# Kernel tuning notes

Hardware: AMD Instinct MI355X
Metric: run time of the kernel (lower is better)

## Reference

```python
import jax, jax.numpy as jnp
import numpy as np

B = 2048


def _maxpool2(x):
    return jax.lax.reduce_window(x, -jnp.inf, jax.lax.max,
                                 (1, 1, 2, 2), (1, 1, 2, 2), 'VALID')


def setup_inputs() -> dict:
    key = jax.random.key(0)
    ks = jax.random.split(key, 7)
    return {
        'x': jax.random.normal(ks[0], (B, 3, 32, 32), dtype=jnp.float32),
        'conv_w': jax.random.normal(ks[1], (45, 1, 5, 5), dtype=jnp.float32),
        'conv_b': jax.random.normal(ks[2], (45,), dtype=jnp.float32) * 0.1,
        'tree_w': jax.random.normal(ks[3], (1, 16, 15, 3, 7, 7, 2, 2), dtype=jnp.float32),
        'tree_b': jax.random.normal(ks[4], (1, 16, 3, 7), dtype=jnp.float32),
        'fc_w': jax.random.normal(ks[5], (10, 336), dtype=jnp.float32),
        'fc_b': jax.random.normal(ks[6], (10,), dtype=jnp.float32) * 0.1,
    }


def reference(x, conv_w, conv_b, tree_w, tree_b, fc_w, fc_b):
    # grouped conv: in=3, groups=3, out=45, kernel 5x5, VALID -> (B,45,28,28)
    out = jax.lax.conv_general_dilated(
        x, conv_w, window_strides=(1, 1), padding='VALID',
        dimension_numbers=('NCHW', 'OIHW', 'NCHW'), feature_group_count=3)
    out = jax.nn.sigmoid(out + conv_b[None, :, None, None])
    out = _maxpool2(out)  # (B,45,14,14)
    b = out.shape[0]
    # unfold((2,2),stride=2) + the torch reshape/transpose chain is equivalent to:
    # (B,45,14,14) -> (b, g=3, m=15, i=7, ki=2, j=7, kj=2) -> (b,m,g,i,j,ki,kj)
    xt = out.reshape(b, 3, 15, 7, 2, 7, 2).transpose(0, 2, 1, 3, 5, 4, 6)
    # TreeLayer: elementwise mul with weights (16,m,g,i,j,ki,kj) then sum over m,j,ki,kj
    t = jnp.einsum('bmgijkl,fmgijkl->bfgi', xt, tree_w[0]) + tree_b  # (B,16,3,7)
    t = jax.nn.sigmoid(t)
    return t.reshape(b, 16 * 3 * 7) @ fc_w.T + fc_b  # (B,10)
```

## Files before the change

kernel.cpp:

```cpp
#include <hip/hip_runtime.h>
#include <hip/hip_fp16.h>

#define BATCH 2048
#define NPREP 95

typedef _Float16 f16x8 __attribute__((ext_vector_type(8)));
typedef float f32x4 __attribute__((ext_vector_type(4)));

__device__ __forceinline__ float sigmoidf(float v) {
    return 1.0f / (1.0f + __expf(-v));
}

#define WS_W3B  0
#define WS_FCW  301056
#define WS_PS   322560
#define PS_G_STRIDE (7u * 2048u * 448u)

__global__ __launch_bounds__(256, 8) void kA_conv_prep(
    const float* __restrict__ x,
    const float* __restrict__ conv_w,
    const float* __restrict__ conv_b,
    const float* __restrict__ tree_w,
    const float* __restrict__ fc_w,
    ushort* __restrict__ W3B,
    float* __restrict__ FCW,
    ushort* __restrict__ ps3)
{
    __shared__ __align__(16) ushort xsc[2 * 4656];
    const int tid = threadIdx.x;

    if (blockIdx.x < NPREP) {
        int pidx = blockIdx.x * 256 + tid;
        if (pidx < 18816) {
            int gi = pidx / 896;
            int rem = pidx - gi * 896;
            int c = rem >> 6, lane2 = rem & 63;
            int f = lane2 & 15, qq = lane2 >> 4;
            int g = gi / 7, i = gi - g * 7;
            ushort h[8];
            #pragma unroll
            for (int u = 0; u < 8; u++) {
                int k = c * 32 + qq * 8 + u;
                int tt = k >> 6;
                int q2 = (k >> 4) & 3;
                int nn = k & 15;
                int u27 = tt * 4 + q2;
                int ki = u27 / 14;
                int pw = u27 - ki * 14;
                int j = pw >> 1, kj = pw & 1;
                float v = 0.f;
                if (nn < 15)
                    v = tree_w[(size_t)f * 8820 + nn * 588 + g * 196 + i * 28
                               + j * 4 + ki * 2 + kj];
                h[u] = __half_as_ushort(__float2half(v));
            }
            *(uint4*)(W3B + (size_t)pidx * 8) = *(uint4*)h;
        } else if (pidx < 24192) {
            int j = pidx - 18816;
            int f = j & 15, o = (j >> 4) & 15, gi = j >> 8;
            FCW[j] = (o < 10) ? fc_w[o * 336 + f * 21 + gi] : 0.f;
        }
        return;
    }

    const int blk2 = blockIdx.x - NPREP;
    const int pair = blk2 / 3;
    const int g    = blk2 - pair * 3;
    const int img0 = pair * 2;
    const int lane = tid & 63;
    const int n    = lane & 15;
    const int q    = lane >> 4;
    const int wave = tid >> 6;

    #pragma unroll
    for (int im2 = 0; im2 < 2; im2++) {
        float4 v = ((const float4*)(x + (size_t)(img0 + im2) * 3072 + g * 1024))[tid];
        int row = tid >> 3, col = (tid & 7) * 4;
        __half2 a = __float22half2_rn(make_float2(v.x, v.y));
        __half2 b = __float22half2_rn(make_float2(v.z, v.w));
        uint2 pk;
        pk.x = *(unsigned int*)&a;
        pk.y = *(unsigned int*)&b;
        *(uint2*)(xsc + im2 * 4656 + row * 36 + col) = pk;
    }
    if (tid < 64) {
        int im2 = tid >> 5, r = tid & 31;
        *(uint2*)(xsc + im2 * 4656 + r * 36 + 32) = make_uint2(0u, 0u);
    }

    f16x8 B1 = {0, 0, 0, 0, 0, 0, 0, 0};
    f16x8 B2 = {0, 0, 0, 0, 0, 0, 0, 0};
    float bias = 0.f;
    if (n < 15) {
        const float* wrow = conv_w + (g * 15 + n) * 25;
        #pragma unroll
        for (int u = 0; u < 5; u++) B1[u] = (_Float16)wrow[q * 5 + u];
        if (q == 0) {
            #pragma unroll
            for (int u = 0; u < 5; u++) B2[u] = (_Float16)wrow[20 + u];
        }
        bias = conv_b[g * 15 + n];
    }
    __syncthreads();

    for (int t = tid; t < 1728; t += 256) {
        int im2 = t / 864;
        int rem = t - im2 * 864;
        int s = rem / 288 + 1;
        int rem2 = rem - (s - 1) * 288;
        int row = rem2 / 9, g4 = rem2 - row * 9;
        ushort* base = xsc + im2 * 4656;
        ushort* dst = base + s * 1164 + row * 36 + g4 * 4;
        if (g4 == 8) { *(uint2*)dst = make_uint2(0u, 0u); continue; }
        uint2 lo = *(const uint2*)(base + row * 36 + g4 * 4);
        uint2 hi = *(const uint2*)(base + row * 36 + g4 * 4 + 4);
        unsigned int w0 = lo.x, w1 = lo.y, w2 = hi.x, w3 = hi.y;
        unsigned int o0, o1;
        if (s == 1)      { o0 = (w0 >> 16) | (w1 << 16); o1 = (w1 >> 16) | (w2 << 16); }
        else if (s == 2) { o0 = w1;                      o1 = w2; }
        else             { o0 = (w1 >> 16) | (w2 << 16); o1 = (w2 >> 16) | (w3 << 16); }
        *(uint2*)dst = make_uint2(o0, o1);
    }

    const int dr = (n >> 1) & 1, dc = n & 1, n4 = n >> 2;
    const int a2c = 144 - q * 36;
    int aoff[13], svr[13];
    #pragma unroll
    for (int it = 0; it < 13; it++) {
        int t = wave + it * 4;
        int pb = t * 4 + n4;
        int ph = pb / 14, pw = pb - ph * 14;
        int r = 2 * ph + dr, c = 2 * pw + dc;
        int s = c & 3;
        aoff[it] = s * 1164 + (r + q) * 36 + (c - s);
        int i = t / 7, tt = t - i * 7;
        svr[it] = i * (2048 * 448) + tt * 64 + lane;
    }
    __syncthreads();

    ushort* psg = ps3 + (size_t)g * PS_G_STRIDE;
    #pragma unroll
    for (int im2 = 0; im2 < 2; im2++) {
        const ushort* xb = xsc + im2 * 4656;
        const int sb = (img0 + im2) * 448;
        #pragma unroll
        for (int it = 0; it < 12; it++) {
            const ushort* pA = xb + aoff[it];
            union { struct { uint2 a, b; } u; f16x8 v; } A1, A2;
            A1.u.a = *(const uint2*)pA;
            A1.u.b = *(const uint2*)(pA + 4);
            A2.u.a = *(const uint2*)(pA + a2c);
            A2.u.b = *(const uint2*)(pA + a2c + 4);
            f32x4 d = {0.f, 0.f, 0.f, 0.f};
            d = __builtin_amdgcn_mfma_f32_16x16x32_f16(A1.v, B1, d, 0, 0, 0);
            d = __builtin_amdgcn_mfma_f32_16x16x32_f16(A2.v, B2, d, 0, 0, 0);
            float mx = fmaxf(fmaxf(d[0], d[1]), fmaxf(d[2], d[3]));
            float val = (n < 15) ? sigmoidf(mx + bias) : 0.f;
            psg[sb + svr[it]] = __half_as_ushort(__float2half(val));
        }
        if (wave == 0) {
            const ushort* pA = xb + aoff[12];
            union { struct { uint2 a, b; } u; f16x8 v; } A1, A2;
            A1.u.a = *(const uint2*)pA;
            A1.u.b = *(const uint2*)(pA + 4);
            A2.u.a = *(const uint2*)(pA + a2c);
            A2.u.b = *(const uint2*)(pA + a2c + 4);
            f32x4 d = {0.f, 0.f, 0.f, 0.f};
            d = __builtin_amdgcn_mfma_f32_16x16x32_f16(A1.v, B1, d, 0, 0, 0);
            d = __builtin_amdgcn_mfma_f32_16x16x32_f16(A2.v, B2, d, 0, 0, 0);
            float mx = fmaxf(fmaxf(d[0], d[1]), fmaxf(d[2], d[3]));
            float val = (n < 15) ? sigmoidf(mx + bias) : 0.f;
            psg[sb + svr[12]] = __half_as_ushort(__float2half(val));
        }
    }
}

__global__ __launch_bounds__(128, 3) void kBC_tree_fc(
    const ushort* __restrict__ ps3,
    const ushort* __restrict__ W3B,
    const float* __restrict__ tree_b,
    const float* __restrict__ FCW,
    const float* __restrict__ fc_b,
    float* __restrict__ out)
{
    __shared__ __align__(16) ushort im[32 * 456];
    __shared__ __align__(16) ushort tsl[32 * 16];

    const int btile = blockIdx.x;
    const int gi    = blockIdx.y;
    const int img0  = btile * 32;
    const int tid   = threadIdx.x;
    const int lane  = tid & 63;
    const int n     = lane & 15;
    const int q     = lane >> 4;
    const int wave  = tid >> 6;

    const uint4* src = (const uint4*)(ps3 + ((size_t)gi * 2048 + img0) * 448);
    #pragma unroll
    for (int it = 0; it < 14; it++) {
        int t = tid + it * 128;
        int img = t / 56;
        int o = t - img * 56;
        *(uint4*)(im + img * 456 + o * 8) = src[t];
    }

    const f16x8* Wbase = (const f16x8*)W3B + (size_t)gi * 896;
    f16x8 B[14];
    #pragma unroll
    for (int c = 0; c < 14; c++) B[c] = Wbase[c * 64 + lane];
    __syncthreads();

    f32x4 D = {0.f, 0.f, 0.f, 0.f};
    const ushort* arow = im + (wave * 16 + n) * 456;
    #pragma unroll
    for (int c = 0; c < 14; c++) {
        f16x8 Af = *(const f16x8*)(arow + c * 32 + q * 8);
        D = __builtin_amdgcn_mfma_f32_16x16x32_f16(Af, B[c], D, 0, 0, 0);
    }

    float bias = tree_b[n * 21 + gi];
    #pragma unroll
    for (int r = 0; r < 4; r++) {
        int imgL = wave * 16 + q * 4 + r;
        tsl[imgL * 16 + n] = __half_as_ushort(__float2half(sigmoidf(D[r] + bias)));
    }
    __syncthreads();

    const float4* Wfc = (const float4*)(FCW + gi * 256);
    for (int t = tid; t < 320; t += 128) {
        int img = t / 10, o = t - (t / 10) * 10;
        const uint4* tp = (const uint4*)(tsl + img * 16);
        uint4 t0 = tp[0], t1 = tp[1];
        const __half2* h = (const __half2*)&t0;
        const __half2* h2 = (const __half2*)&t1;
        float4 w0 = Wfc[o * 4], w1 = Wfc[o * 4 + 1];
        float4 w2 = Wfc[o * 4 + 2], w3 = Wfc[o * 4 + 3];
        float acc = (gi == 0) ? fc_b[o] : 0.f;
        float2 p;
        p = __half22float2(h[0]);  acc = fmaf(p.x, w0.x, acc); acc = fmaf(p.y, w0.y, acc);
        p = __half22float2(h[1]);  acc = fmaf(p.x, w0.z, acc); acc = fmaf(p.y, w0.w, acc);
        p = __half22float2(h[2]);  acc = fmaf(p.x, w1.x, acc); acc = fmaf(p.y, w1.y, acc);
        p = __half22float2(h[3]);  acc = fmaf(p.x, w1.z, acc); acc = fmaf(p.y, w1.w, acc);
        p = __half22float2(h2[0]); acc = fmaf(p.x, w2.x, acc); acc = fmaf(p.y, w2.y, acc);
        p = __half22float2(h2[1]); acc = fmaf(p.x, w2.z, acc); acc = fmaf(p.y, w2.w, acc);
        p = __half22float2(h2[2]); acc = fmaf(p.x, w3.x, acc); acc = fmaf(p.y, w3.y, acc);
        p = __half22float2(h2[3]); acc = fmaf(p.x, w3.z, acc); acc = fmaf(p.y, w3.w, acc);
#if defined(__HIP_PLATFORM_AMD__)
        unsafeAtomicAdd(out + (size_t)(img0 + img) * 10 + o, acc);
#else
        atomicAdd(out + (size_t)(img0 + img) * 10 + o, acc);
#endif
    }
}

extern "C" void kernel_launch(void* const* d_in, const int* in_sizes, int n_in,
                              void* d_out, int out_size, void* d_ws, size_t ws_size,
                              hipStream_t stream) {
    const float* x      = (const float*)d_in[0];
    const float* conv_w = (const float*)d_in[1];
    const float* conv_b = (const float*)d_in[2];
    const float* tree_w = (const float*)d_in[3];
    const float* tree_b = (const float*)d_in[4];
    const float* fc_w   = (const float*)d_in[5];
    const float* fc_b   = (const float*)d_in[6];
    float* out = (float*)d_out;

    ushort* W3B = (ushort*)((char*)d_ws + WS_W3B);
    float*  FCW = (float*)((char*)d_ws + WS_FCW);
    ushort* ps3 = (ushort*)((char*)d_ws + WS_PS);

    hipMemsetAsync(out, 0, (size_t)BATCH * 10 * sizeof(float), stream);
    kA_conv_prep<<<NPREP + 1024 * 3, 256, 0, stream>>>(x, conv_w, conv_b, tree_w,
                                                       fc_w, W3B, FCW, ps3);
    kBC_tree_fc<<<dim3(64, 21), 128, 0, stream>>>(ps3, W3B, tree_b, FCW, fc_b, out);
}
```

Baseline: 123.2 us.

## Fuse conv, tree layer and FC into one kernel via shared memory

```diff
diff --git a/kernel.cpp b/kernel.cpp
--- a/kernel.cpp
+++ b/kernel.cpp
@@ -2,7 +2,6 @@
 #include <hip/hip_fp16.h>
 
 #define BATCH 2048
-#define NPREP 95
 
 typedef _Float16 f16x8 __attribute__((ext_vector_type(8)));
 typedef float f32x4 __attribute__((ext_vector_type(4)));
@@ -13,59 +12,68 @@
 
 #define WS_W3B  0
 #define WS_FCW  301056
-#define WS_PS   322560
-#define PS_G_STRIDE (7u * 2048u * 448u)
-
-__global__ __launch_bounds__(256, 8) void kA_conv_prep(
+
+__global__ __launch_bounds__(256) void k_prep(
+    const float* __restrict__ tree_w,
+    const float* __restrict__ fc_w,
+    ushort* __restrict__ W3B,
+    float* __restrict__ FCW2)
+{
+    int pidx = blockIdx.x * 256 + threadIdx.x;
+    if (pidx < 18816) {
+        int gi = pidx / 896;
+        int rem = pidx - gi * 896;
+        int c = rem >> 6, lane2 = rem & 63;
+        int f = lane2 & 15, qq = lane2 >> 4;
+        int g = gi / 7, i = gi - g * 7;
+        ushort h[8];
+        #pragma unroll
+        for (int u = 0; u < 8; u++) {
+            int k = c * 32 + qq * 8 + u;
+            int tt = k >> 6;
+            int q2 = (k >> 4) & 3;
+            int nn = k & 15;
+            int u27 = tt * 4 + q2;
+            int ki = u27 / 14;
+            int pw = u27 - ki * 14;
+            int j = pw >> 1, kj = pw & 1;
+            float v = 0.f;
+            if (nn < 15)
+                v = tree_w[(size_t)f * 8820 + nn * 588 + g * 196 + i * 28
+                           + j * 4 + ki * 2 + kj];
+            h[u] = __half_as_ushort(__float2half(v));
+        }
+        *(uint4*)(W3B + (size_t)pidx * 8) = *(uint4*)h;
+    } else if (pidx < 22176) {
+        int j = pidx - 18816;
+        int f = j & 15;
+        int r = j >> 4;
+        int i = r % 7;
+        int r2 = r / 7;
+        int o = r2 % 10;
+        int g = r2 / 10;
+        FCW2[j] = fc_w[o * 336 + f * 21 + g * 7 + i];
+    }
+}
+
+__global__ __launch_bounds__(256, 4) void kF_all(
     const float* __restrict__ x,
     const float* __restrict__ conv_w,
     const float* __restrict__ conv_b,
-    const float* __restrict__ tree_w,
-    const float* __restrict__ fc_w,
-    ushort* __restrict__ W3B,
-    float* __restrict__ FCW,
-    ushort* __restrict__ ps3)
+    const ushort* __restrict__ W3B,
+    const float* __restrict__ FCW2,
+    const float* __restrict__ tree_b,
+    const float* __restrict__ fc_b,
+    float* __restrict__ out)
 {
     __shared__ __align__(16) ushort xsc[2 * 4656];
-    const int tid = threadIdx.x;
-
-    if (blockIdx.x < NPREP) {
-        int pidx = blockIdx.x * 256 + tid;
-        if (pidx < 18816) {
-            int gi = pidx / 896;
-            int rem = pidx - gi * 896;
-            int c = rem >> 6, lane2 = rem & 63;
-            int f = lane2 & 15, qq = lane2 >> 4;
-            int g = gi / 7, i = gi - g * 7;
-            ushort h[8];
-            #pragma unroll
-            for (int u = 0; u < 8; u++) {
-                int k = c * 32 + qq * 8 + u;
-                int tt = k >> 6;
-                int q2 = (k >> 4) & 3;
-                int nn = k & 15;
-                int u27 = tt * 4 + q2;
-                int ki = u27 / 14;
-                int pw = u27 - ki * 14;
-                int j = pw >> 1, kj = pw & 1;
-                float v = 0.f;
-                if (nn < 15)
-                    v = tree_w[(size_t)f * 8820 + nn * 588 + g * 196 + i * 28
-                               + j * 4 + ki * 2 + kj];
-                h[u] = __half_as_ushort(__float2half(v));
-            }
-            *(uint4*)(W3B + (size_t)pidx * 8) = *(uint4*)h;
-        } else if (pidx < 24192) {
-            int j = pidx - 18816;
-            int f = j & 15, o = (j >> 4) & 15, gi = j >> 8;
-            FCW[j] = (o < 10) ? fc_w[o * 336 + f * 21 + gi] : 0.f;
-        }
-        return;
-    }
-
-    const int blk2 = blockIdx.x - NPREP;
-    const int pair = blk2 / 3;
-    const int g    = blk2 - pair * 3;
+    __shared__ __align__(16) ushort ps[2 * 3192];
+    __shared__ __align__(16) ushort tsl[14 * 16];
+
+    const int tid  = threadIdx.x;
+    const int blk  = blockIdx.x;
+    const int pair = blk / 3;
+    const int g    = blk - pair * 3;
     const int img0 = pair * 2;
     const int lane = tid & 63;
     const int n    = lane & 15;
@@ -134,15 +142,14 @@
         int s = c & 3;
         aoff[it] = s * 1164 + (r + q) * 36 + (c - s);
         int i = t / 7, tt = t - i * 7;
-        svr[it] = i * (2048 * 448) + tt * 64 + lane;
-    }
-    __syncthreads();
-
-    ushort* psg = ps3 + (size_t)g * PS_G_STRIDE;
+        svr[it] = i * 456 + tt * 64 + lane;
+    }
+    __syncthreads();
+
     #pragma unroll
     for (int im2 = 0; im2 < 2; im2++) {
         const ushort* xb = xsc + im2 * 4656;
-        const int sb = (img0 + im2) * 448;
+        ushort* pso = ps + im2 * 3192;
         #pragma unroll
         for (int it = 0; it < 12; it++) {
             const ushort* pA = xb + aoff[it];
@@ -156,7 +163,7 @@
             d = __builtin_amdgcn_mfma_f32_16x16x32_f16(A2.v, B2, d, 0, 0, 0);
             float mx = fmaxf(fmaxf(d[0], d[1]), fmaxf(d[2], d[3]));
             float val = (n < 15) ? sigmoidf(mx + bias) : 0.f;
-            psg[sb + svr[it]] = __half_as_ushort(__float2half(val));
+            pso[svr[it]] = __half_as_ushort(__float2half(val));
         }
         if (wave == 0) {
             const ushort* pA = xb + aoff[12];
@@ -170,85 +177,50 @@
             d = __builtin_amdgcn_mfma_f32_16x16x32_f16(A2.v, B2, d, 0, 0, 0);
             float mx = fmaxf(fmaxf(d[0], d[1]), fmaxf(d[2], d[3]));
             float val = (n < 15) ? sigmoidf(mx + bias) : 0.f;
-            psg[sb + svr[12]] = __half_as_ushort(__float2half(val));
-        }
-    }
-}
-
-__global__ __launch_bounds__(128, 3) void kBC_tree_fc(
-    const ushort* __restrict__ ps3,
-    const ushort* __restrict__ W3B,
-    const float* __restrict__ tree_b,
-    const float* __restrict__ FCW,
-    const float* __restrict__ fc_b,
-    float* __restrict__ out)
-{
-    __shared__ __align__(16) ushort im[32 * 456];
-    __shared__ __align__(16) ushort tsl[32 * 16];
-
-    const int btile = blockIdx.x;
-    const int gi    = blockIdx.y;
-    const int img0  = btile * 32;
-    const int tid   = threadIdx.x;
-    const int lane  = tid & 63;
-    const int n     = lane & 15;
-    const int q     = lane >> 4;
-    const int wave  = tid >> 6;
-
-    const uint4* src = (const uint4*)(ps3 + ((size_t)gi * 2048 + img0) * 448);
-    #pragma unroll
-    for (int it = 0; it < 14; it++) {
-        int t = tid + it * 128;
-        int img = t / 56;
-        int o = t - img * 56;
-        *(uint4*)(im + img * 456 + o * 8) = src[t];
-    }
-
-    const f16x8* Wbase = (const f16x8*)W3B + (size_t)gi * 896;
-    f16x8 B[14];
-    #pragma unroll
-    for (int c = 0; c < 14; c++) B[c] = Wbase[c * 64 + lane];
-    __syncthreads();
-
-    f32x4 D = {0.f, 0.f, 0.f, 0.f};
-    const ushort* arow = im + (wave * 16 + n) * 456;
-    #pragma unroll
-    for (int c = 0; c < 14; c++) {
-        f16x8 Af = *(const f16x8*)(arow + c * 32 + q * 8);
-        D = __builtin_amdgcn_mfma_f32_16x16x32_f16(Af, B[c], D, 0, 0, 0);
-    }
-
-    float bias = tree_b[n * 21 + gi];
-    #pragma unroll
-    for (int r = 0; r < 4; r++) {
-        int imgL = wave * 16 + q * 4 + r;
-        tsl[imgL * 16 + n] = __half_as_ushort(__float2half(sigmoidf(D[r] + bias)));
-    }
-    __syncthreads();
-
-    const float4* Wfc = (const float4*)(FCW + gi * 256);
-    for (int t = tid; t < 320; t += 128) {
-        int img = t / 10, o = t - (t / 10) * 10;
-        const uint4* tp = (const uint4*)(tsl + img * 16);
-        uint4 t0 = tp[0], t1 = tp[1];
-        const __half2* h = (const __half2*)&t0;
-        const __half2* h2 = (const __half2*)&t1;
-        float4 w0 = Wfc[o * 4], w1 = Wfc[o * 4 + 1];
-        float4 w2 = Wfc[o * 4 + 2], w3 = Wfc[o * 4 + 3];
-        float acc = (gi == 0) ? fc_b[o] : 0.f;
-        float2 p;
-        p = __half22float2(h[0]);  acc = fmaf(p.x, w0.x, acc); acc = fmaf(p.y, w0.y, acc);
-        p = __half22float2(h[1]);  acc = fmaf(p.x, w0.z, acc); acc = fmaf(p.y, w0.w, acc);
-        p = __half22float2(h[2]);  acc = fmaf(p.x, w1.x, acc); acc = fmaf(p.y, w1.y, acc);
-        p = __half22float2(h[3]);  acc = fmaf(p.x, w1.z, acc); acc = fmaf(p.y, w1.w, acc);
-        p = __half22float2(h2[0]); acc = fmaf(p.x, w2.x, acc); acc = fmaf(p.y, w2.y, acc);
-        p = __half22float2(h2[1]); acc = fmaf(p.x, w2.z, acc); acc = fmaf(p.y, w2.w, acc);
-        p = __half22float2(h2[2]); acc = fmaf(p.x, w3.x, acc); acc = fmaf(p.y, w3.y, acc);
-        p = __half22float2(h2[3]); acc = fmaf(p.x, w3.z, acc); acc = fmaf(p.y, w3.w, acc);
+            pso[svr[12]] = __half_as_ushort(__float2half(val));
+        }
+    }
+    __syncthreads();
+
+    for (int ii = wave; ii < 7; ii += 4) {
+        const f16x8* Wb = (const f16x8*)W3B + (size_t)(g * 7 + ii) * 896;
+        const ushort* ap = ps + (lane & 1) * 3192 + ii * 456;
+        f32x4 D = {0.f, 0.f, 0.f, 0.f};
+        #pragma unroll
+        for (int c = 0; c < 14; c++) {
+            f16x8 Af = *(const f16x8*)(ap + c * 32 + q * 8);
+            f16x8 Bf = Wb[c * 64 + lane];
+            D = __builtin_amdgcn_mfma_f32_16x16x32_f16(Af, Bf, D, 0, 0, 0);
+        }
+        if (q == 0) {
+            float tb = tree_b[n * 21 + g * 7 + ii];
+            tsl[(0 * 7 + ii) * 16 + n] =
+                __half_as_ushort(__float2half(sigmoidf(D[0] + tb)));
+            tsl[(1 * 7 + ii) * 16 + n] =
+                __half_as_ushort(__float2half(sigmoidf(D[1] + tb)));
+        }
+    }
+    __syncthreads();
+
+    if (wave == 0 && lane < 20) {
+        int im2 = lane / 10, o = lane - (lane / 10) * 10;
+        const __half2* tp = (const __half2*)(tsl + im2 * 7 * 16);
+        const float4* wp = (const float4*)(FCW2 + (size_t)(g * 10 + o) * 112);
+        float acc = (g == 0) ? fc_b[o] : 0.f;
+        #pragma unroll
+        for (int jj = 0; jj < 28; jj++) {
+            float4 w4 = wp[jj];
+            float2 p0 = __half22float2(tp[2 * jj]);
+            float2 p1 = __half22float2(tp[2 * jj + 1]);
+            acc = fmaf(p0.x, w4.x, acc);
+            acc = fmaf(p0.y, w4.y, acc);
+            acc = fmaf(p1.x, w4.z, acc);
+            acc = fmaf(p1.y, w4.w, acc);
+        }
 #if defined(__HIP_PLATFORM_AMD__)
-        unsafeAtomicAdd(out + (size_t)(img0 + img) * 10 + o, acc);
+        unsafeAtomicAdd(out + (size_t)(img0 + im2) * 10 + o, acc);
 #else
-        atomicAdd(out + (size_t)(img0 + img) * 10 + o, acc);
+        atomicAdd(out + (size_t)(img0 + im2) * 10 + o, acc);
 #endif
     }
 }
@@ -265,12 +237,11 @@
     const float* fc_b   = (const float*)d_in[6];
     float* out = (float*)d_out;
 
-    ushort* W3B = (ushort*)((char*)d_ws + WS_W3B);
-    float*  FCW = (float*)((char*)d_ws + WS_FCW);
-    ushort* ps3 = (ushort*)((char*)d_ws + WS_PS);
+    ushort* W3B  = (ushort*)((char*)d_ws + WS_W3B);
+    float*  FCW2 = (float*)((char*)d_ws + WS_FCW);
 
     hipMemsetAsync(out, 0, (size_t)BATCH * 10 * sizeof(float), stream);
-    kA_conv_prep<<<NPREP + 1024 * 3, 256, 0, stream>>>(x, conv_w, conv_b, tree_w,
-                                                       fc_w, W3B, FCW, ps3);
-    kBC_tree_fc<<<dim3(64, 21), 128, 0, stream>>>(ps3, W3B, tree_b, FCW, fc_b, out);
-}
+    k_prep<<<87, 256, 0, stream>>>(tree_w, fc_w, W3B, FCW2);
+    kF_all<<<1024 * 3, 256, 0, stream>>>(x, conv_w, conv_b, W3B, FCW2,
+                                         tree_b, fc_b, out);
+}
```

After: 115.3 us. 1.07x faster.
